# Kernel optimization log

Measured on AMD Instinct MI355X. Metric: run time of the kernel, lower is better.

Reference implementation:

```python
import jax, jax.numpy as jnp
import numpy as np

B, D, U = 256, 2048, 2048  # batch, input_dim, units
EPS = 1e-8


def setup_inputs() -> dict:
    key = jax.random.key(0)
    ks = jax.random.split(key, 20)
    sd = 1.0 / np.sqrt(D)
    su = 1.0 / np.sqrt(U)
    inp = {
        'x': jax.random.normal(ks[0], (B, D), jnp.float32),
        'h_prev': jax.random.normal(ks[1], (B, U), jnp.float32),
        'c_prev': jax.random.normal(ks[2], (B, U), jnp.float32),
        'n_prev': jax.random.uniform(ks[3], (B, U), jnp.float32),
        'm_prev': jax.random.normal(ks[4], (B, U), jnp.float32),
        # input-to-gate weights (Dense with bias), keras layout [in, out]
        'Wz': jax.random.normal(ks[5], (D, U), jnp.float32) * sd,
        'Wi': jax.random.normal(ks[6], (D, U), jnp.float32) * sd,
        'Wf': jax.random.normal(ks[7], (D, U), jnp.float32) * sd,
        'Wo': jax.random.normal(ks[8], (D, U), jnp.float32) * sd,
        'bz': jnp.zeros((U,), jnp.float32),
        'bi': jnp.zeros((U,), jnp.float32),
        'bf': jnp.zeros((U,), jnp.float32),
        'bo': jnp.zeros((U,), jnp.float32),
        # recurrent weights (Dense without bias)
        'Uz': jax.random.normal(ks[9], (U, U), jnp.float32) * su,
        'Ui': jax.random.normal(ks[10], (U, U), jnp.float32) * su,
        'Uf': jax.random.normal(ks[11], (U, U), jnp.float32) * su,
        'Uo': jax.random.normal(ks[12], (U, U), jnp.float32) * su,
    }
    return inp


def reference(x, h_prev, c_prev, n_prev, m_prev,
              Wz, Wi, Wf, Wo, bz, bi, bf, bo, Uz, Ui, Uf, Uo):
    # fuse the 8 small GEMMs into 2 wide GEMMs (same math, gates split after)
    W = jnp.concatenate([Wz, Wi, Wf, Wo], axis=1)      # [D, 4U]
    Uc = jnp.concatenate([Uz, Ui, Uf, Uo], axis=1)     # [U, 4U]
    b = jnp.concatenate([bz, bi, bf, bo], axis=0)      # [4U]
    pre = x @ W + h_prev @ Uc + b                      # [B, 4U]
    z_tilde, i_tilde, f_tilde, o_tilde = jnp.split(pre, 4, axis=1)

    # exponential-gate stabilization (forget_gate_type='exponential')
    m_t = jnp.maximum(i_tilde + m_prev, i_tilde)
    i_t = jnp.exp(i_tilde - m_t)
    f_t = jnp.exp(f_tilde + m_prev - m_t)

    o_t = jax.nn.sigmoid(o_tilde)
    z_t = jnp.tanh(z_tilde)

    c_t = f_t * c_prev + i_t * z_t
    n_t = f_t * n_prev + i_t
    h_t = o_t * (c_t / (n_t + EPS))
    return jnp.stack([h_t, c_t, n_t, m_t], axis=0)  # [4, B, U]
```

## Files before the change

### kernel.cpp

```cpp
#include <hip/hip_runtime.h>
#include <cstdint>
#include <cstddef>

#define B_    256
#define D_    2048
#define U_    2048
#define NTOT  8192
#define BN    32
#define BK    128
#define KSLICE 2048
#define CHUNKS (KSLICE / BK)
#define BPITCH 136

typedef _Float16 half8 __attribute__((ext_vector_type(8)));
typedef float floatx16 __attribute__((ext_vector_type(16)));

__global__ __launch_bounds__(256) void prep_kernel(
    const float* __restrict__ x, const float* __restrict__ h,
    _Float16* __restrict__ Ahi)
{
    int gid   = blockIdx.x * 256 + threadIdx.x;
    int koct  = gid >> 8;
    int row   = gid & 255;
    int col0  = koct * 8;
    const float* src = (col0 < D_) ? (x + row * D_ + col0)
                                   : (h + row * U_ + (col0 - D_));
    float4 v0 = *(const float4*)(src);
    float4 v1 = *(const float4*)(src + 4);
    float v[8] = {v0.x, v0.y, v0.z, v0.w, v1.x, v1.y, v1.z, v1.w};
    half8 hi;
#pragma unroll
    for (int i = 0; i < 8; ++i) hi[i] = (_Float16)v[i];
    *(half8*)(Ahi + (koct * 256 + row) * 8) = hi;
}

__global__ __launch_bounds__(256) void gemm_kernel(
    const _Float16* __restrict__ Ahi,
    const float* __restrict__ Wz, const float* __restrict__ Wi,
    const float* __restrict__ Wf, const float* __restrict__ Wo,
    const float* __restrict__ Uz, const float* __restrict__ Ui,
    const float* __restrict__ Uf, const float* __restrict__ Uo,
    float* __restrict__ P)
{
    __shared__ __align__(16) _Float16 sB[2][BN * BPITCH];

    const int t    = threadIdx.x;
    const int w    = t >> 6;
    const int lane = t & 63;
    const int lg   = lane >> 5;
    const int lm   = lane & 31;

    const int ntile = blockIdx.x;
    const int ks    = blockIdx.y;
    const int n0    = ntile * BN;
    const int g     = n0 >> 11;
    const int c0    = n0 & (U_ - 1);
    const int koctB = ks * 256;

    const float* wsel[8] = {Wz, Wi, Wf, Wo, Uz, Ui, Uf, Uo};
    const float* Bm   = wsel[ks * 4 + g];
    const float* Bcol = Bm + c0 + lm;

    const int bko = w * 2 + lg;

    floatx16 acc[2] = {};
    float breg[2][8];

#define LOAD_B(kk)                                                            \
    {                                                                         \
        _Pragma("unroll")                                                     \
        for (int j = 0; j < 2; ++j) {                                         \
            const float* src = Bcol + (size_t)((kk) * BK + (bko + 8 * j) * 8) * U_; \
            _Pragma("unroll")                                                 \
            for (int i = 0; i < 8; ++i)                                       \
                breg[j][i] = src[(size_t)i * U_];                             \
        }                                                                     \
    }

#define WRITE_B(buf)                                                          \
    {                                                                         \
        _Pragma("unroll")                                                     \
        for (int j = 0; j < 2; ++j) {                                         \
            half8 hb;                                                         \
            _Pragma("unroll")                                                 \
            for (int i = 0; i < 8; ++i) hb[i] = (_Float16)breg[j][i];         \
            *(half8*)(&sB[buf][lm * BPITCH + (bko + 8 * j) * 8]) = hb;        \
        }                                                                     \
    }

    LOAD_B(0);
    WRITE_B(0);
    __syncthreads();

    const int arow0 = w * 64 + lm;

    for (int kk = 0; kk < CHUNKS; ++kk) {
        int cur = kk & 1;
        if (kk + 1 < CHUNKS) LOAD_B(kk + 1);

#pragma unroll
        for (int kstep = 0; kstep < 8; ++kstep) {
            int ko = koctB + kk * 16 + kstep * 2 + lg;
            half8 a0 = *(const half8*)(Ahi + ((size_t)ko * 256 + arow0) * 8);
            half8 a1 = *(const half8*)(Ahi + ((size_t)ko * 256 + arow0 + 32) * 8);
            half8 b  = *(const half8*)(&sB[cur][lm * BPITCH + kstep * 16 + lg * 8]);
            acc[0] = __builtin_amdgcn_mfma_f32_32x32x16_f16(a0, b, acc[0], 0, 0, 0);
            acc[1] = __builtin_amdgcn_mfma_f32_32x32x16_f16(a1, b, acc[1], 0, 0, 0);
        }
        if (kk + 1 < CHUNKS) WRITE_B(cur ^ 1);
        __syncthreads();
    }
#undef LOAD_B
#undef WRITE_B

    float* Pks = P + (size_t)ks * ((size_t)B_ * NTOT);
#pragma unroll
    for (int mt = 0; mt < 2; ++mt)
#pragma unroll
        for (int r = 0; r < 16; ++r) {
            int m = w * 64 + mt * 32 + 4 * lg + (r & 3) + 8 * (r >> 2);
            Pks[(size_t)m * NTOT + n0 + lm] = acc[mt][r];
        }
}

__global__ __launch_bounds__(256) void gates_kernel(
    const float* __restrict__ P,
    const float* __restrict__ c_prev, const float* __restrict__ n_prev,
    const float* __restrict__ m_prev,
    const float* __restrict__ bz, const float* __restrict__ bi,
    const float* __restrict__ bf, const float* __restrict__ bo,
    float* __restrict__ out)
{
    const size_t PS = (size_t)B_ * NTOT;
    const int OS = B_ * U_;
    int gid = blockIdx.x * 256 + threadIdx.x;
    int m = gid >> 9;
    int u = (gid & 511) * 4;

    float pre[4][4];
#pragma unroll
    for (int gi = 0; gi < 4; ++gi) {
        const float* base = P + (size_t)m * NTOT + gi * U_ + u;
        float4 s0 = *(const float4*)(base);
        float4 s1 = *(const float4*)(base + PS);
        pre[gi][0] = s0.x + s1.x;
        pre[gi][1] = s0.y + s1.y;
        pre[gi][2] = s0.z + s1.z;
        pre[gi][3] = s0.w + s1.w;
    }
    float4 bzv = *(const float4*)(bz + u);
    float4 biv = *(const float4*)(bi + u);
    float4 bfv = *(const float4*)(bf + u);
    float4 bov = *(const float4*)(bo + u);
    float bza[4] = {bzv.x, bzv.y, bzv.z, bzv.w};
    float bia[4] = {biv.x, biv.y, biv.z, biv.w};
    float bfa[4] = {bfv.x, bfv.y, bfv.z, bfv.w};
    float boa[4] = {bov.x, bov.y, bov.z, bov.w};

    float4 cp4 = *(const float4*)(c_prev + m * U_ + u);
    float4 np4 = *(const float4*)(n_prev + m * U_ + u);
    float4 mp4 = *(const float4*)(m_prev + m * U_ + u);
    float cpa[4] = {cp4.x, cp4.y, cp4.z, cp4.w};
    float npa[4] = {np4.x, np4.y, np4.z, np4.w};
    float mpa[4] = {mp4.x, mp4.y, mp4.z, mp4.w};

    float hr[4], cr[4], nr[4], mr[4];
#pragma unroll
    for (int e = 0; e < 4; ++e) {
        float zt = pre[0][e] + bza[e];
        float it = pre[1][e] + bia[e];
        float ft = pre[2][e] + bfa[e];
        float ot = pre[3][e] + boa[e];
        float mp = mpa[e];
        float m_t = fmaxf(it + mp, it);
        float i_t = expf(it - m_t);
        float f_t = expf(ft + mp - m_t);
        float o_t = 1.0f / (1.0f + expf(-ot));
        float z_t = tanhf(zt);
        float c_t = f_t * cpa[e] + i_t * z_t;
        float n_t = f_t * npa[e] + i_t;
        float h_t = o_t * (c_t / (n_t + 1e-8f));
        hr[e] = h_t; cr[e] = c_t; nr[e] = n_t; mr[e] = m_t;
    }
    float4 hv = {hr[0], hr[1], hr[2], hr[3]};
    float4 cv = {cr[0], cr[1], cr[2], cr[3]};
    float4 nv = {nr[0], nr[1], nr[2], nr[3]};
    float4 mv = {mr[0], mr[1], mr[2], mr[3]};
    *(float4*)(out + 0 * OS + m * U_ + u) = hv;
    *(float4*)(out + 1 * OS + m * U_ + u) = cv;
    *(float4*)(out + 2 * OS + m * U_ + u) = nv;
    *(float4*)(out + 3 * OS + m * U_ + u) = mv;
}

extern "C" void kernel_launch(void* const* d_in, const int* in_sizes, int n_in,
                              void* d_out, int out_size, void* d_ws, size_t ws_size,
                              hipStream_t stream)
{
    const float* x  = (const float*)d_in[0];
    const float* h  = (const float*)d_in[1];
    const float* cp = (const float*)d_in[2];
    const float* np = (const float*)d_in[3];
    const float* mp = (const float*)d_in[4];
    const float* Wz = (const float*)d_in[5];
    const float* Wi = (const float*)d_in[6];
    const float* Wf = (const float*)d_in[7];
    const float* Wo = (const float*)d_in[8];
    const float* bz = (const float*)d_in[9];
    const float* bi = (const float*)d_in[10];
    const float* bf = (const float*)d_in[11];
    const float* bo = (const float*)d_in[12];
    const float* Uz = (const float*)d_in[13];
    const float* Ui = (const float*)d_in[14];
    const float* Uf = (const float*)d_in[15];
    const float* Uo = (const float*)d_in[16];

    float* P = (float*)d_ws;
    _Float16* Ahi = (_Float16*)((char*)d_ws + (size_t)2 * B_ * NTOT * sizeof(float));

    prep_kernel<<<512, 256, 0, stream>>>(x, h, Ahi);
    gemm_kernel<<<dim3(256, 2), 256, 0, stream>>>(Ahi,
        Wz, Wi, Wf, Wo, Uz, Ui, Uf, Uo, P);
    gates_kernel<<<512, 256, 0, stream>>>(P, cp, np, mp, bz, bi, bf, bo,
        (float*)d_out);
}
```

Measured before the change: 218.5 us.

## Widen GEMM N-tile to 128, stage A in LDS via async loads, split-K by 4

Each GEMM block now covers 128 output columns instead of 32, so every A fragment it loads feeds four MFMA column tiles. The A operand is staged into LDS with global_load_lds and double-buffered alongside B, replacing per-wave direct global reads. K is split four ways so the grid has enough blocks, which adds two more partial-sum planes that gates_kernel must read and sum. The aim is less redundant global A traffic and a higher MFMA-to-load ratio, at the cost of more LDS per block, fewer blocks, and extra partial-sum memory traffic.

After: 218.0 us. About the same (-0.2%).

```diff
diff --git a/kernel.cpp b/kernel.cpp
--- a/kernel.cpp
+++ b/kernel.cpp
@@ -2,15 +2,16 @@
 #include <cstdint>
 #include <cstddef>
 
-#define B_    256
-#define D_    2048
-#define U_    2048
-#define NTOT  8192
-#define BN    32
-#define BK    128
-#define KSLICE 2048
+#define B_     256
+#define D_     2048
+#define U_     2048
+#define NTOT   8192
+#define BN     128
+#define BK     64
+#define KS     4
+#define KSLICE 1024
 #define CHUNKS (KSLICE / BK)
-#define BPITCH 136
+#define BPITCH 72
 
 typedef _Float16 half8 __attribute__((ext_vector_type(8)));
 typedef float floatx16 __attribute__((ext_vector_type(16)));
@@ -42,6 +43,7 @@
     const float* __restrict__ Uf, const float* __restrict__ Uo,
     float* __restrict__ P)
 {
+    __shared__ __align__(16) _Float16 sA[2][8 * 256 * 8];
     __shared__ __align__(16) _Float16 sB[2][BN * BPITCH];
 
     const int t    = threadIdx.x;
@@ -55,22 +57,37 @@
     const int n0    = ntile * BN;
     const int g     = n0 >> 11;
     const int c0    = n0 & (U_ - 1);
-    const int koctB = ks * 256;
+    const int krow0 = (ks & 1) * KSLICE;
+    const int koctB = ks * 128;
 
     const float* wsel[8] = {Wz, Wi, Wf, Wo, Uz, Ui, Uf, Uo};
-    const float* Bm   = wsel[ks * 4 + g];
-    const float* Bcol = Bm + c0 + lm;
-
-    const int bko = w * 2 + lg;
-
-    floatx16 acc[2] = {};
-    float breg[2][8];
+    const float* Bm = wsel[(ks >> 1) * 4 + g];
+
+    const int colT = (w & 1) * 64 + lane;
+    const int koT  = w >> 1;
+    const float* Bcol = Bm + (size_t)krow0 * U_ + c0 + colT;
+
+    floatx16 acc[2][4] = {};
+    float breg[4][8];
+
+#define ISSUE_A(kk, buf)                                                      \
+    {                                                                         \
+        _Pragma("unroll")                                                     \
+        for (int j = 0; j < 8; ++j) {                                         \
+            int idx  = j * 256 + t;                                           \
+            size_t gidx = ((size_t)(koctB + (kk) * 8) * 256 + idx) * 8;       \
+            __builtin_amdgcn_global_load_lds(                                 \
+                (const __attribute__((address_space(1))) void*)(Ahi + gidx),  \
+                (__attribute__((address_space(3))) void*)(&sA[buf][idx * 8]), \
+                16, 0, 0);                                                    \
+        }                                                                     \
+    }
 
 #define LOAD_B(kk)                                                            \
     {                                                                         \
         _Pragma("unroll")                                                     \
-        for (int j = 0; j < 2; ++j) {                                         \
-            const float* src = Bcol + (size_t)((kk) * BK + (bko + 8 * j) * 8) * U_; \
+        for (int j = 0; j < 4; ++j) {                                         \
+            const float* src = Bcol + (size_t)((kk) * BK + (koT + 2 * j) * 8) * U_; \
             _Pragma("unroll")                                                 \
             for (int i = 0; i < 8; ++i)                                       \
                 breg[j][i] = src[(size_t)i * U_];                             \
@@ -80,36 +97,49 @@
 #define WRITE_B(buf)                                                          \
     {                                                                         \
         _Pragma("unroll")                                                     \
-        for (int j = 0; j < 2; ++j) {                                         \
+        for (int j = 0; j < 4; ++j) {                                         \
             half8 hb;                                                         \
             _Pragma("unroll")                                                 \
             for (int i = 0; i < 8; ++i) hb[i] = (_Float16)breg[j][i];         \
-            *(half8*)(&sB[buf][lm * BPITCH + (bko + 8 * j) * 8]) = hb;        \
+            *(half8*)(&sB[buf][colT * BPITCH + (koT + 2 * j) * 8]) = hb;      \
         }                                                                     \
     }
 
+    ISSUE_A(0, 0);
     LOAD_B(0);
     WRITE_B(0);
     __syncthreads();
 
-    const int arow0 = w * 64 + lm;
-
     for (int kk = 0; kk < CHUNKS; ++kk) {
         int cur = kk & 1;
-        if (kk + 1 < CHUNKS) LOAD_B(kk + 1);
-
-#pragma unroll
-        for (int kstep = 0; kstep < 8; ++kstep) {
-            int ko = koctB + kk * 16 + kstep * 2 + lg;
-            half8 a0 = *(const half8*)(Ahi + ((size_t)ko * 256 + arow0) * 8);
-            half8 a1 = *(const half8*)(Ahi + ((size_t)ko * 256 + arow0 + 32) * 8);
-            half8 b  = *(const half8*)(&sB[cur][lm * BPITCH + kstep * 16 + lg * 8]);
-            acc[0] = __builtin_amdgcn_mfma_f32_32x32x16_f16(a0, b, acc[0], 0, 0, 0);
-            acc[1] = __builtin_amdgcn_mfma_f32_32x32x16_f16(a1, b, acc[1], 0, 0, 0);
+        if (kk + 1 < CHUNKS) {
+            ISSUE_A(kk + 1, cur ^ 1);
+            LOAD_B(kk + 1);
+        }
+#pragma unroll
+        for (int kstep = 0; kstep < 4; ++kstep) {
+            half8 a[2], b[4];
+#pragma unroll
+            for (int mt = 0; mt < 2; ++mt) {
+                int row = w * 64 + mt * 32 + lm;
+                a[mt] = *(const half8*)(&sA[cur][((kstep * 2 + lg) * 256 + row) * 8]);
+            }
+#pragma unroll
+            for (int nt = 0; nt < 4; ++nt) {
+                int col = nt * 32 + lm;
+                b[nt] = *(const half8*)(&sB[cur][col * BPITCH + kstep * 16 + lg * 8]);
+            }
+#pragma unroll
+            for (int mt = 0; mt < 2; ++mt)
+#pragma unroll
+                for (int nt = 0; nt < 4; ++nt)
+                    acc[mt][nt] = __builtin_amdgcn_mfma_f32_32x32x16_f16(
+                        a[mt], b[nt], acc[mt][nt], 0, 0, 0);
         }
         if (kk + 1 < CHUNKS) WRITE_B(cur ^ 1);
         __syncthreads();
     }
+#undef ISSUE_A
 #undef LOAD_B
 #undef WRITE_B
 
@@ -117,9 +147,13 @@
 #pragma unroll
     for (int mt = 0; mt < 2; ++mt)
 #pragma unroll
-        for (int r = 0; r < 16; ++r) {
-            int m = w * 64 + mt * 32 + 4 * lg + (r & 3) + 8 * (r >> 2);
-            Pks[(size_t)m * NTOT + n0 + lm] = acc[mt][r];
+        for (int nt = 0; nt < 4; ++nt) {
+            int n = n0 + nt * 32 + lm;
+#pragma unroll
+            for (int r = 0; r < 16; ++r) {
+                int m = w * 64 + mt * 32 + 4 * lg + (r & 3) + 8 * (r >> 2);
+                Pks[(size_t)m * NTOT + n] = acc[mt][nt][r];
+            }
         }
 }
 
@@ -143,10 +177,12 @@
         const float* base = P + (size_t)m * NTOT + gi * U_ + u;
         float4 s0 = *(const float4*)(base);
         float4 s1 = *(const float4*)(base + PS);
-        pre[gi][0] = s0.x + s1.x;
-        pre[gi][1] = s0.y + s1.y;
-        pre[gi][2] = s0.z + s1.z;
-        pre[gi][3] = s0.w + s1.w;
+        float4 s2 = *(const float4*)(base + 2 * PS);
+        float4 s3 = *(const float4*)(base + 3 * PS);
+        pre[gi][0] = s0.x + s1.x + s2.x + s3.x;
+        pre[gi][1] = s0.y + s1.y + s2.y + s3.y;
+        pre[gi][2] = s0.z + s1.z + s2.z + s3.z;
+        pre[gi][3] = s0.w + s1.w + s2.w + s3.w;
     }
     float4 bzv = *(const float4*)(bz + u);
     float4 biv = *(const float4*)(bi + u);
@@ -215,10 +251,10 @@
     const float* Uo = (const float*)d_in[16];
 
     float* P = (float*)d_ws;
-    _Float16* Ahi = (_Float16*)((char*)d_ws + (size_t)2 * B_ * NTOT * sizeof(float));
+    _Float16* Ahi = (_Float16*)((char*)d_ws + (size_t)4 * B_ * NTOT * sizeof(float));
 
     prep_kernel<<<512, 256, 0, stream>>>(x, h, Ahi);
-    gemm_kernel<<<dim3(256, 2), 256, 0, stream>>>(Ahi,
+    gemm_kernel<<<dim3(64, 4), 256, 0, stream>>>(Ahi,
         Wz, Wi, Wf, Wo, Uz, Ui, Uf, Uo, P);
     gates_kernel<<<512, 256, 0, stream>>>(P, cp, np, mp, bz, bi, bf, bo,
         (float*)d_out);
```

## Give each wave a full-M column strip with 8-way split-K in registers

Applied to the files above, without the earlier changes.

The GEMM is restructured so that each wavefront owns a 32-column strip for all 256 rows and a 512-deep K slice, with 8 K-splits instead of 2. The shared-memory B staging and block barriers are removed: B is converted to fp16 in registers and A fragments are loaded straight from global memory, double-buffered in registers. Partial sums are stored as fp16 to shrink the larger split-K workspace, and the gates kernel reduces all 8 partials. This trades more register pressure, eight times more A reads per wave, and lower precision of the partials for the removal of LDS traffic and synchronisation and for higher parallelism.

Measured after the change: 548.5 us. 151% more time.

```diff
diff --git a/kernel.cpp b/kernel.cpp
--- a/kernel.cpp
+++ b/kernel.cpp
@@ -2,17 +2,16 @@
 #include <cstdint>
 #include <cstddef>
 
-#define B_    256
-#define D_    2048
-#define U_    2048
-#define NTOT  8192
-#define BN    32
-#define BK    128
-#define KSLICE 2048
-#define CHUNKS (KSLICE / BK)
-#define BPITCH 136
+#define B_     256
+#define D_     2048
+#define U_     2048
+#define NTOT   8192
+#define KS     8
+#define KSLICE 512
+#define KSTEPS (KSLICE / 16)
 
 typedef _Float16 half8 __attribute__((ext_vector_type(8)));
+typedef _Float16 half4 __attribute__((ext_vector_type(4)));
 typedef float floatx16 __attribute__((ext_vector_type(16)));
 
 __global__ __launch_bounds__(256) void prep_kernel(
@@ -34,97 +33,77 @@
     *(half8*)(Ahi + (koct * 256 + row) * 8) = hi;
 }
 
-__global__ __launch_bounds__(256) void gemm_kernel(
+__global__ __launch_bounds__(256, 2) void gemm_kernel(
     const _Float16* __restrict__ Ahi,
     const float* __restrict__ Wz, const float* __restrict__ Wi,
     const float* __restrict__ Wf, const float* __restrict__ Wo,
     const float* __restrict__ Uz, const float* __restrict__ Ui,
     const float* __restrict__ Uf, const float* __restrict__ Uo,
-    float* __restrict__ P)
-{
-    __shared__ __align__(16) _Float16 sB[2][BN * BPITCH];
-
+    _Float16* __restrict__ P)
+{
     const int t    = threadIdx.x;
     const int w    = t >> 6;
     const int lane = t & 63;
     const int lg   = lane >> 5;
     const int lm   = lane & 31;
 
-    const int ntile = blockIdx.x;
-    const int ks    = blockIdx.y;
-    const int n0    = ntile * BN;
+    const int wid   = blockIdx.x * 4 + w;
+    const int strip = wid & 255;
+    const int ks    = wid >> 8;
+    const int n0    = strip * 32;
     const int g     = n0 >> 11;
     const int c0    = n0 & (U_ - 1);
-    const int koctB = ks * 256;
+    const int krow0 = (ks & 3) * KSLICE;
+    const int koctB = ks * (KSLICE / 8);
 
     const float* wsel[8] = {Wz, Wi, Wf, Wo, Uz, Ui, Uf, Uo};
-    const float* Bm   = wsel[ks * 4 + g];
-    const float* Bcol = Bm + c0 + lm;
-
-    const int bko = w * 2 + lg;
-
-    floatx16 acc[2] = {};
+    const float* Bm = wsel[(ks >> 2) * 4 + g];
+    const float* Bbase = Bm + (size_t)krow0 * U_ + c0 + lm;
+
+    floatx16 acc[8] = {};
+
     float breg[2][8];
-
-#define LOAD_B(kk)                                                            \
+    half8 areg[2][8];
+
+#define LOADK(kk, buf)                                                        \
     {                                                                         \
+        const float* bp = Bbase + (size_t)((kk) * 16 + lg * 8) * U_;          \
         _Pragma("unroll")                                                     \
-        for (int j = 0; j < 2; ++j) {                                         \
-            const float* src = Bcol + (size_t)((kk) * BK + (bko + 8 * j) * 8) * U_; \
-            _Pragma("unroll")                                                 \
-            for (int i = 0; i < 8; ++i)                                       \
-                breg[j][i] = src[(size_t)i * U_];                             \
-        }                                                                     \
-    }
-
-#define WRITE_B(buf)                                                          \
-    {                                                                         \
+        for (int j = 0; j < 8; ++j) breg[buf][j] = bp[(size_t)j * U_];        \
+        const _Float16* ap =                                                  \
+            Ahi + ((size_t)(koctB + (kk) * 2 + lg) * 256 + lm) * 8;           \
         _Pragma("unroll")                                                     \
-        for (int j = 0; j < 2; ++j) {                                         \
-            half8 hb;                                                         \
-            _Pragma("unroll")                                                 \
-            for (int i = 0; i < 8; ++i) hb[i] = (_Float16)breg[j][i];         \
-            *(half8*)(&sB[buf][lm * BPITCH + (bko + 8 * j) * 8]) = hb;        \
-        }                                                                     \
-    }
-
-    LOAD_B(0);
-    WRITE_B(0);
-    __syncthreads();
-
-    const int arow0 = w * 64 + lm;
-
-    for (int kk = 0; kk < CHUNKS; ++kk) {
+        for (int mt = 0; mt < 8; ++mt)                                        \
+            areg[buf][mt] = *(const half8*)(ap + mt * 32 * 8);                \
+    }
+
+    LOADK(0, 0);
+
+    for (int kk = 0; kk < KSTEPS; ++kk) {
         int cur = kk & 1;
-        if (kk + 1 < CHUNKS) LOAD_B(kk + 1);
-
-#pragma unroll
-        for (int kstep = 0; kstep < 8; ++kstep) {
-            int ko = koctB + kk * 16 + kstep * 2 + lg;
-            half8 a0 = *(const half8*)(Ahi + ((size_t)ko * 256 + arow0) * 8);
-            half8 a1 = *(const half8*)(Ahi + ((size_t)ko * 256 + arow0 + 32) * 8);
-            half8 b  = *(const half8*)(&sB[cur][lm * BPITCH + kstep * 16 + lg * 8]);
-            acc[0] = __builtin_amdgcn_mfma_f32_32x32x16_f16(a0, b, acc[0], 0, 0, 0);
-            acc[1] = __builtin_amdgcn_mfma_f32_32x32x16_f16(a1, b, acc[1], 0, 0, 0);
+        if (kk + 1 < KSTEPS) LOADK(kk + 1, cur ^ 1);
+        half8 b;
+#pragma unroll
+        for (int j = 0; j < 8; ++j) b[j] = (_Float16)breg[cur][j];
+#pragma unroll
+        for (int mt = 0; mt < 8; ++mt)
+            acc[mt] = __builtin_amdgcn_mfma_f32_32x32x16_f16(
+                areg[cur][mt], b, acc[mt], 0, 0, 0);
+    }
+#undef LOADK
+
+    _Float16* Pks = P + (size_t)ks * ((size_t)B_ * NTOT);
+#pragma unroll
+    for (int mt = 0; mt < 8; ++mt)
+#pragma unroll
+        for (int r = 0; r < 16; ++r) {
+            int m = mt * 32 + 4 * lg + (r & 3) + 8 * (r >> 2);
+            Pks[(size_t)m * NTOT + n0 + lm] = (_Float16)acc[mt][r];
         }
-        if (kk + 1 < CHUNKS) WRITE_B(cur ^ 1);
-        __syncthreads();
-    }
-#undef LOAD_B
-#undef WRITE_B
-
-    float* Pks = P + (size_t)ks * ((size_t)B_ * NTOT);
-#pragma unroll
-    for (int mt = 0; mt < 2; ++mt)
-#pragma unroll
-        for (int r = 0; r < 16; ++r) {
-            int m = w * 64 + mt * 32 + 4 * lg + (r & 3) + 8 * (r >> 2);
-            Pks[(size_t)m * NTOT + n0 + lm] = acc[mt][r];
-        }
 }
 
 __global__ __launch_bounds__(256) void gates_kernel(
-    const float* __restrict__ P,
+    const _Float16* __restrict__ P,
     const float* __restrict__ c_prev, const float* __restrict__ n_prev,
     const float* __restrict__ m_prev,
     const float* __restrict__ bz, const float* __restrict__ bi,
@@ -140,13 +119,16 @@
     float pre[4][4];
 #pragma unroll
     for (int gi = 0; gi < 4; ++gi) {
-        const float* base = P + (size_t)m * NTOT + gi * U_ + u;
-        float4 s0 = *(const float4*)(base);
-        float4 s1 = *(const float4*)(base + PS);
-        pre[gi][0] = s0.x + s1.x;
-        pre[gi][1] = s0.y + s1.y;
-        pre[gi][2] = s0.z + s1.z;
-        pre[gi][3] = s0.w + s1.w;
+        const _Float16* base = P + (size_t)m * NTOT + gi * U_ + u;
+        float s[4] = {0.f, 0.f, 0.f, 0.f};
+#pragma unroll
+        for (int sp = 0; sp < KS; ++sp) {
+            half4 v = *(const half4*)(base + sp * PS);
+            s[0] += (float)v[0]; s[1] += (float)v[1];
+            s[2] += (float)v[2]; s[3] += (float)v[3];
+        }
+        pre[gi][0] = s[0]; pre[gi][1] = s[1];
+        pre[gi][2] = s[2]; pre[gi][3] = s[3];
     }
     float4 bzv = *(const float4*)(bz + u);
     float4 biv = *(const float4*)(bi + u);
@@ -214,11 +196,11 @@
     const float* Uf = (const float*)d_in[15];
     const float* Uo = (const float*)d_in[16];
 
-    float* P = (float*)d_ws;
-    _Float16* Ahi = (_Float16*)((char*)d_ws + (size_t)2 * B_ * NTOT * sizeof(float));
+    _Float16* P = (_Float16*)d_ws;
+    _Float16* Ahi = (_Float16*)((char*)d_ws + (size_t)KS * B_ * NTOT * sizeof(_Float16));
 
     prep_kernel<<<512, 256, 0, stream>>>(x, h, Ahi);
-    gemm_kernel<<<dim3(256, 2), 256, 0, stream>>>(Ahi,
+    gemm_kernel<<<512, 256, 0, stream>>>(Ahi,
         Wz, Wi, Wf, Wo, Uz, Ui, Uf, Uo, P);
     gates_kernel<<<512, 256, 0, stream>>>(P, cp, np, mp, bz, bi, bf, bo,
         (float*)d_out);
```
